# Kernel optimization log

Hardware: AMD Instinct MI355X
Metric: run time of the kernel (lower is better)

Reference implementation:

```python
import jax, jax.numpy as jnp
import numpy as np
from jax import lax

B, T, N_INPUT = 64, 2048, 257
HIDDEN = 32
N_OUTPUT = 10


def setup_inputs() -> dict:
    key = jax.random.key(0)
    ks = jax.random.split(key, 7)
    return {
        "specs": jax.random.normal(ks[0], (B, T, N_INPUT), dtype=jnp.float32),
        "W_ih": jax.random.normal(ks[1], (4 * HIDDEN, N_INPUT), dtype=jnp.float32) * 0.05,
        "W_hh": jax.random.normal(ks[2], (4 * HIDDEN, HIDDEN), dtype=jnp.float32) * 0.05,
        "b_ih": jax.random.normal(ks[3], (4 * HIDDEN,), dtype=jnp.float32) * 0.05,
        "b_hh": jax.random.normal(ks[4], (4 * HIDDEN,), dtype=jnp.float32) * 0.05,
        "W_out": jax.random.normal(ks[5], (N_OUTPUT, HIDDEN), dtype=jnp.float32) * 0.05,
        "b_out": jax.random.normal(ks[6], (N_OUTPUT,), dtype=jnp.float32) * 0.05,
    }


def reference(specs, W_ih, W_hh, b_ih, b_hh, W_out, b_out):
    # specs: [B, T, n_input]. PyTorch LSTMCell, gate order (i, f, g, o).
    b, t, _ = specs.shape
    h0 = jnp.zeros((b, HIDDEN), dtype=specs.dtype)
    c0 = jnp.zeros((b, HIDDEN), dtype=specs.dtype)
    # Precompute input projection for all timesteps in one GEMM: [B, T, 4H]
    x_proj = jnp.einsum("bti,gi->btg", specs, W_ih) + b_ih + b_hh
    x_proj = jnp.swapaxes(x_proj, 0, 1)  # [T, B, 4H] for scan

    def step(carry, xg):
        h, c = carry
        gates = xg + h @ W_hh.T  # [B, 4H]
        i, f, g, o = jnp.split(gates, 4, axis=-1)
        i = jax.nn.sigmoid(i)
        f = jax.nn.sigmoid(f)
        g = jnp.tanh(g)
        o = jax.nn.sigmoid(o)
        c = f * c + i * g
        h = o * jnp.tanh(c)
        return (h, c), None

    (hn, _), _ = lax.scan(step, (h0, c0), x_proj)
    logits = jax.nn.relu(hn) @ W_out.T + b_out  # [B, n_output]
    return jax.nn.log_softmax(logits, axis=1)
```

## Files before the change

kernel.cpp:

```cpp
#include <hip/hip_runtime.h>

#define B_SZ 64
#define T_LEN 2048
#define NIN 257
#define HID 32
#define G4 128
#define NOUT 10

#define TBT 128
#define PAD 34
#define CH 8
#define NSCAN 64
#define NGEMMP 128
#define NTILE 1024
#define TPB 16

typedef int v2i __attribute__((ext_vector_type(2)));
typedef unsigned long long u64;

__device__ __forceinline__ void pkfma2(float2& acc, float2 w, u64 h2) {
  asm("v_pk_fma_f32 %0, %1, %2, %0" : "+v"(acc) : "v"(w), "s"(h2));
}

__device__ __forceinline__ float2 pkadd(float2 a, float2 b) {
  float2 d;
  asm("v_pk_add_f32 %0, %1, %2" : "=v"(d) : "v"(a), "v"(b));
  return d;
}

#define LDP(a0, b0, PB, OA, OB) \
  asm volatile("global_load_dword %0, %2, off offset:" OA "\n\t" \
               "global_load_dword %1, %2, off offset:" OB \
               : "=&v"(a0), "=&v"(b0) : "v"(PB))

#define LOAD_CHUNK(Aa, Bb, PB) do { \
  LDP(Aa[0], Bb[0], PB, "0",    "256");  \
  LDP(Aa[1], Bb[1], PB, "512",  "768");  \
  LDP(Aa[2], Bb[2], PB, "1024", "1280"); \
  LDP(Aa[3], Bb[3], PB, "1536", "1792"); \
  LDP(Aa[4], Bb[4], PB, "2048", "2304"); \
  LDP(Aa[5], Bb[5], PB, "2560", "2816"); \
  LDP(Aa[6], Bb[6], PB, "3072", "3328"); \
  LDP(Aa[7], Bb[7], PB, "3584", "3840"); \
} while (0)

#define WAIT16() do { asm volatile("s_waitcnt vmcnt(16)" ::: "memory"); \
                      __builtin_amdgcn_sched_barrier(0); } while (0)
#define WAIT0()  do { asm volatile("s_waitcnt vmcnt(0)" ::: "memory"); \
                      __builtin_amdgcn_sched_barrier(0); } while (0)

__device__ __forceinline__ void gemm_tile(
    const float* __restrict__ A, const float* __restrict__ W,
    const float* __restrict__ b_ih, const float* __restrict__ b_hh,
    float* __restrict__ C, int bt0, float* sA, float* sB)
{
  const int tid = threadIdx.x;
  const int gt = tid & 15;
  const int btt = tid >> 4;
  float acc[8][8];
#pragma unroll
  for (int i = 0; i < 8; ++i)
#pragma unroll
    for (int j = 0; j < 8; ++j) acc[i][j] = 0.f;

  for (int kc = 0; kc < 8; ++kc) {
    const int k0 = kc * 32;
    __syncthreads();
#pragma unroll
    for (int i = 0; i < 16; ++i) {
      int s = i * 256 + tid;
      int r = s >> 5, cc = s & 31;
      sA[r * PAD + cc] = A[(size_t)(bt0 + r) * NIN + k0 + cc];
      sB[r * PAD + cc] = W[(size_t)r * NIN + k0 + cc];
    }
    __syncthreads();
#pragma unroll
    for (int k2 = 0; k2 < 16; ++k2) {
      float2 a2[8], b2[8];
#pragma unroll
      for (int i = 0; i < 8; ++i)
        a2[i] = *(const float2*)&sA[(btt + 16 * i) * PAD + 2 * k2];
#pragma unroll
      for (int j = 0; j < 8; ++j)
        b2[j] = *(const float2*)&sB[(gt + 16 * j) * PAD + 2 * k2];
#pragma unroll
      for (int i = 0; i < 8; ++i)
#pragma unroll
        for (int j = 0; j < 8; ++j) {
          acc[i][j] = fmaf(a2[i].x, b2[j].x, acc[i][j]);
          acc[i][j] = fmaf(a2[i].y, b2[j].y, acc[i][j]);
        }
    }
  }
  {
    float a[8], bb[8];
#pragma unroll
    for (int i = 0; i < 8; ++i) a[i] = A[(size_t)(bt0 + btt + 16 * i) * NIN + 256];
#pragma unroll
    for (int j = 0; j < 8; ++j) bb[j] = W[(size_t)(gt + 16 * j) * NIN + 256];
#pragma unroll
    for (int i = 0; i < 8; ++i)
#pragma unroll
      for (int j = 0; j < 8; ++j) acc[i][j] += a[i] * bb[j];
  }
  float bias[8];
#pragma unroll
  for (int j = 0; j < 8; ++j) bias[j] = b_ih[gt + 16 * j] + b_hh[gt + 16 * j];
#pragma unroll
  for (int i = 0; i < 8; ++i) {
    size_t row = (size_t)(bt0 + btt + 16 * i) * G4;
#pragma unroll
    for (int j = 0; j < 8; ++j) C[row + gt + 16 * j] = acc[i][j] + bias[j];
  }
}

__global__ __launch_bounds__(256) void fused(
    const float* __restrict__ A,
    const float* __restrict__ W,
    const float* __restrict__ b_ih,
    const float* __restrict__ b_hh,
    const float* __restrict__ W_hh,
    const float* __restrict__ W_out,
    const float* __restrict__ b_out,
    float* __restrict__ out,
    float* __restrict__ xproj,
    int* __restrict__ flags,
    int nowait)
{
  __shared__ float sA[TBT * PAD];
  __shared__ float sB[G4 * PAD];
  const int bid = blockIdx.x;

  if (bid >= NSCAN) {
    const int p = bid - NSCAN;
    for (int idx = p; idx < NTILE; idx += NGEMMP) {
      const int ti = idx >> 6, bb = idx & 63;
      const int bt0 = bb * T_LEN + ti * TBT;
      gemm_tile(A, W, b_ih, b_hh, xproj, bt0, sA, sB);
      __threadfence();
      __syncthreads();
      if (threadIdx.x == 0)
        __hip_atomic_store(&flags[idx], 1, __ATOMIC_RELEASE, __HIP_MEMORY_SCOPE_AGENT);
    }
    return;
  }

  if (threadIdx.x >= 64) return;
  __builtin_amdgcn_s_setprio(3);
  const int b = bid;
  const int l = threadIdx.x;

  float2 wA[16], wB[16];
#pragma unroll
  for (int j = 0; j < 16; j += 2) {
    float4 v0 = *(const float4*)&W_hh[l * HID + 2 * j];
    wA[j]     = make_float2(v0.x, v0.y);
    wA[j + 1] = make_float2(v0.z, v0.w);
    float4 v1 = *(const float4*)&W_hh[(l + 64) * HID + 2 * j];
    wB[j]     = make_float2(v1.x, v1.y);
    wB[j + 1] = make_float2(v1.z, v1.w);
  }
  const float eB  = (l < HID) ? -2.88539008f : -1.44269504f;
  const float mBc = (l < HID) ? 2.f : 1.f;
  const float aBc = (l < HID) ? -1.f : 0.f;

  float c = 0.f, h = 0.f;
  u64 hp[16];
#pragma unroll
  for (int k = 0; k < 16; ++k) hp[k] = 0ull;

  const float* xb = xproj + (size_t)b * T_LEN * G4;

  auto step = [&](float xa, float xg) {
    float2 aA[4], aB[4];
    aA[0] = make_float2(xa, 0.f);
    aB[0] = make_float2(xg, 0.f);
#pragma unroll
    for (int q = 1; q < 4; ++q) {
      aA[q] = make_float2(0.f, 0.f);
      aB[q] = make_float2(0.f, 0.f);
    }
#pragma unroll
    for (int j = 0; j < 16; j += 4) {
#pragma unroll
      for (int q = 0; q < 4; ++q) {
        pkfma2(aA[q], wA[j + q], hp[j + q]);
        pkfma2(aB[q], wB[j + q], hp[j + q]);
      }
    }
    float2 tA = pkadd(pkadd(aA[0], aA[1]), pkadd(aA[2], aA[3]));
    float2 tB = pkadd(pkadd(aB[0], aB[1]), pkadd(aB[2], aB[3]));
    float accA = tA.x + tA.y;
    float accB = tB.x + tB.y;
    float actA = __builtin_amdgcn_rcpf(1.f + __builtin_amdgcn_exp2f(-1.44269504f * accA));
    float sB2  = __builtin_amdgcn_rcpf(1.f + __builtin_amdgcn_exp2f(eB * accB));
    float actB = fmaf(mBc, sB2, aBc);
    float prod = actA * actB;
    v2i sw = __builtin_amdgcn_permlane32_swap(0, __float_as_int(prod), false, false);
    float pr = __int_as_float(sw[0]);
    c = fmaf(actA, c, pr);
    float t  = __builtin_amdgcn_rcpf(1.f + __builtin_amdgcn_exp2f(-2.88539008f * c));
    float o2 = actB + actB;
    h = fmaf(o2, t, -actB);
#pragma unroll
    for (int k = 0; k < 16; ++k) {
      unsigned lo = (unsigned)__builtin_amdgcn_readlane(__float_as_int(h), 32 + 2 * k);
      unsigned hi = (unsigned)__builtin_amdgcn_readlane(__float_as_int(h), 33 + 2 * k);
      hp[k] = (u64)lo | ((u64)hi << 32);
    }
  };

  float A0[CH], B0[CH], A1[CH], B1[CH];
#define STEPS(Aa, Bb) do { _Pragma("unroll") \
  for (int i = 0; i < CH; ++i) step(Aa[i], Bb[i]); } while (0)

  for (int ti = 0; ti < TPB; ++ti) {
    if (!nowait) {
      while (__hip_atomic_load(&flags[ti * 64 + b], __ATOMIC_ACQUIRE,
                               __HIP_MEMORY_SCOPE_AGENT) == 0)
        __builtin_amdgcn_s_sleep(2);
    }
    const float* pb = xb + (size_t)ti * TBT * G4 + l;
    LOAD_CHUNK(A0, B0, pb); pb += CH * G4;
    LOAD_CHUNK(A1, B1, pb); pb += CH * G4;
#pragma unroll 1
    for (int pc = 0; pc < 7; ++pc) {
      WAIT16();
      STEPS(A0, B0);
      LOAD_CHUNK(A0, B0, pb); pb += CH * G4;
      WAIT16();
      STEPS(A1, B1);
      LOAD_CHUNK(A1, B1, pb); pb += CH * G4;
    }
    WAIT16();
    STEPS(A0, B0);
    WAIT0();
    STEPS(A1, B1);
  }

  float hf[HID];
#pragma unroll
  for (int k = 0; k < HID; ++k)
    hf[k] = __int_as_float(__builtin_amdgcn_readlane(__float_as_int(h), 32 + k));
  float logit = 0.f;
  if (l < NOUT) {
    logit = b_out[l];
#pragma unroll
    for (int j = 0; j < HID; ++j) logit += fmaxf(hf[j], 0.f) * W_out[l * HID + j];
  }
  float m = -1e30f;
#pragma unroll
  for (int n = 0; n < NOUT; ++n) m = fmaxf(m, __shfl(logit, n));
  float s = 0.f;
#pragma unroll
  for (int n = 0; n < NOUT; ++n)
    s += __builtin_amdgcn_exp2f(1.44269504089f * (__shfl(logit, n) - m));
  if (l < NOUT)
    out[b * NOUT + l] = logit - m - 0.69314718056f * __builtin_amdgcn_logf(s);
}

__global__ __launch_bounds__(256) void xproj_gemm(
    const float* __restrict__ A, const float* __restrict__ W,
    const float* __restrict__ b_ih, const float* __restrict__ b_hh,
    float* __restrict__ C)
{
  __shared__ float sA[TBT * PAD];
  __shared__ float sB[G4 * PAD];
  const int idx = blockIdx.x;
  const int ti = idx >> 6, bb = idx & 63;
  gemm_tile(A, W, b_ih, b_hh, C, bb * T_LEN + ti * TBT, sA, sB);
}

extern "C" void kernel_launch(void* const* d_in, const int* in_sizes, int n_in,
                              void* d_out, int out_size, void* d_ws, size_t ws_size,
                              hipStream_t stream) {
  const float* specs = (const float*)d_in[0];
  const float* W_ih  = (const float*)d_in[1];
  const float* W_hh  = (const float*)d_in[2];
  const float* b_ih  = (const float*)d_in[3];
  const float* b_hh  = (const float*)d_in[4];
  const float* W_out = (const float*)d_in[5];
  const float* b_out = (const float*)d_in[6];
  float* outp  = (float*)d_out;
  float* xproj = (float*)d_ws;
  const size_t xbytes = (size_t)B_SZ * T_LEN * G4 * 4;

  if (ws_size >= xbytes + NTILE * sizeof(int)) {
    int* flags = (int*)((char*)d_ws + xbytes);
    (void)hipMemsetAsync(flags, 0, NTILE * sizeof(int), stream);
    fused<<<NSCAN + NGEMMP, 256, 0, stream>>>(specs, W_ih, b_ih, b_hh, W_hh,
                                              W_out, b_out, outp, xproj, flags, 0);
  } else {
    xproj_gemm<<<NTILE, 256, 0, stream>>>(specs, W_ih, b_ih, b_hh, xproj);
    fused<<<NSCAN, 256, 0, stream>>>(specs, W_ih, b_ih, b_hh, W_hh,
                                     W_out, b_out, outp, xproj, (int*)xproj , 1);
  }
}
```

Baseline: 571.8 us.

## Prescale gate preactivations and interleave xproj layout for float2 loads

The GEMM epilogue now multiplies each gate column by its sigmoid/tanh exp2 scale and stores columns interleaved so each scan lane reads its two gate values with one float2 load. The recurrent weights are prescaled the same way, which removes the per-step multiplies and the select-based tanh fixup and rewrites the cell update algebraically. The hand-written inline-asm load pipeline with explicit vmcnt waits is replaced by plain C++ double-buffered loads. The compiler may now schedule the loads and waits less tightly than the hand-tuned asm on the serial critical path.

```diff
diff --git a/kernel.cpp b/kernel.cpp
--- a/kernel.cpp
+++ b/kernel.cpp
@@ -15,6 +15,9 @@
 #define NTILE 1024
 #define TPB 16
 
+#define SC_SIG  -1.44269504f
+#define SC_TANH -2.88539008f
+
 typedef int v2i __attribute__((ext_vector_type(2)));
 typedef unsigned long long u64;
 
@@ -27,27 +30,6 @@
   asm("v_pk_add_f32 %0, %1, %2" : "=v"(d) : "v"(a), "v"(b));
   return d;
 }
-
-#define LDP(a0, b0, PB, OA, OB) \
-  asm volatile("global_load_dword %0, %2, off offset:" OA "\n\t" \
-               "global_load_dword %1, %2, off offset:" OB \
-               : "=&v"(a0), "=&v"(b0) : "v"(PB))
-
-#define LOAD_CHUNK(Aa, Bb, PB) do { \
-  LDP(Aa[0], Bb[0], PB, "0",    "256");  \
-  LDP(Aa[1], Bb[1], PB, "512",  "768");  \
-  LDP(Aa[2], Bb[2], PB, "1024", "1280"); \
-  LDP(Aa[3], Bb[3], PB, "1536", "1792"); \
-  LDP(Aa[4], Bb[4], PB, "2048", "2304"); \
-  LDP(Aa[5], Bb[5], PB, "2560", "2816"); \
-  LDP(Aa[6], Bb[6], PB, "3072", "3328"); \
-  LDP(Aa[7], Bb[7], PB, "3584", "3840"); \
-} while (0)
-
-#define WAIT16() do { asm volatile("s_waitcnt vmcnt(16)" ::: "memory"); \
-                      __builtin_amdgcn_sched_barrier(0); } while (0)
-#define WAIT0()  do { asm volatile("s_waitcnt vmcnt(0)" ::: "memory"); \
-                      __builtin_amdgcn_sched_barrier(0); } while (0)
 
 __device__ __forceinline__ void gemm_tile(
     const float* __restrict__ A, const float* __restrict__ W,
@@ -103,14 +85,20 @@
 #pragma unroll
       for (int j = 0; j < 8; ++j) acc[i][j] += a[i] * bb[j];
   }
-  float bias[8];
-#pragma unroll
-  for (int j = 0; j < 8; ++j) bias[j] = b_ih[gt + 16 * j] + b_hh[gt + 16 * j];
+  float bias[8], sc[8];
+  int off[8];
+#pragma unroll
+  for (int j = 0; j < 8; ++j) {
+    const int col = gt + 16 * j;
+    bias[j] = b_ih[col] + b_hh[col];
+    sc[j] = ((col >> 5) == 2) ? SC_TANH : SC_SIG;
+    off[j] = ((col & 63) << 1) + (col >> 6);
+  }
 #pragma unroll
   for (int i = 0; i < 8; ++i) {
     size_t row = (size_t)(bt0 + btt + 16 * i) * G4;
 #pragma unroll
-    for (int j = 0; j < 8; ++j) C[row + gt + 16 * j] = acc[i][j] + bias[j];
+    for (int j = 0; j < 8; ++j) C[row + off[j]] = (acc[i][j] + bias[j]) * sc[j];
   }
 }
 
@@ -150,26 +138,24 @@
   const int b = bid;
   const int l = threadIdx.x;
 
+  const float wsB = (l < HID) ? SC_TANH : SC_SIG;
   float2 wA[16], wB[16];
 #pragma unroll
   for (int j = 0; j < 16; j += 2) {
     float4 v0 = *(const float4*)&W_hh[l * HID + 2 * j];
-    wA[j]     = make_float2(v0.x, v0.y);
-    wA[j + 1] = make_float2(v0.z, v0.w);
+    wA[j]     = make_float2(v0.x * SC_SIG, v0.y * SC_SIG);
+    wA[j + 1] = make_float2(v0.z * SC_SIG, v0.w * SC_SIG);
     float4 v1 = *(const float4*)&W_hh[(l + 64) * HID + 2 * j];
-    wB[j]     = make_float2(v1.x, v1.y);
-    wB[j + 1] = make_float2(v1.z, v1.w);
-  }
-  const float eB  = (l < HID) ? -2.88539008f : -1.44269504f;
-  const float mBc = (l < HID) ? 2.f : 1.f;
-  const float aBc = (l < HID) ? -1.f : 0.f;
+    wB[j]     = make_float2(v1.x * wsB, v1.y * wsB);
+    wB[j + 1] = make_float2(v1.z * wsB, v1.w * wsB);
+  }
 
   float c = 0.f, h = 0.f;
   u64 hp[16];
 #pragma unroll
   for (int k = 0; k < 16; ++k) hp[k] = 0ull;
 
-  const float* xb = xproj + (size_t)b * T_LEN * G4;
+  const float2* xb2 = (const float2*)(xproj + (size_t)b * T_LEN * G4);
 
   auto step = [&](float xa, float xg) {
     float2 aA[4], aB[4];
@@ -192,16 +178,16 @@
     float2 tB = pkadd(pkadd(aB[0], aB[1]), pkadd(aB[2], aB[3]));
     float accA = tA.x + tA.y;
     float accB = tB.x + tB.y;
-    float actA = __builtin_amdgcn_rcpf(1.f + __builtin_amdgcn_exp2f(-1.44269504f * accA));
-    float sB2  = __builtin_amdgcn_rcpf(1.f + __builtin_amdgcn_exp2f(eB * accB));
-    float actB = fmaf(mBc, sB2, aBc);
-    float prod = actA * actB;
+    float actA = __builtin_amdgcn_rcpf(1.f + __builtin_amdgcn_exp2f(accA));
+    float sB2  = __builtin_amdgcn_rcpf(1.f + __builtin_amdgcn_exp2f(accB));
+    float actA2 = actA + actA;
+    float prod  = fmaf(actA2, sB2, -actA);
     v2i sw = __builtin_amdgcn_permlane32_swap(0, __float_as_int(prod), false, false);
     float pr = __int_as_float(sw[0]);
     c = fmaf(actA, c, pr);
-    float t  = __builtin_amdgcn_rcpf(1.f + __builtin_amdgcn_exp2f(-2.88539008f * c));
-    float o2 = actB + actB;
-    h = fmaf(o2, t, -actB);
+    float t  = __builtin_amdgcn_rcpf(1.f + __builtin_amdgcn_exp2f(SC_TANH * c));
+    float s2 = sB2 + sB2;
+    h = fmaf(s2, t, -sB2);
 #pragma unroll
     for (int k = 0; k < 16; ++k) {
       unsigned lo = (unsigned)__builtin_amdgcn_readlane(__float_as_int(h), 32 + 2 * k);
@@ -210,9 +196,11 @@
     }
   };
 
-  float A0[CH], B0[CH], A1[CH], B1[CH];
-#define STEPS(Aa, Bb) do { _Pragma("unroll") \
-  for (int i = 0; i < CH; ++i) step(Aa[i], Bb[i]); } while (0)
+  float2 X0[CH], X1[CH];
+#define LOADC2(X, P) do { _Pragma("unroll") \
+  for (int i = 0; i < CH; ++i) X[i] = (P)[i * 64]; } while (0)
+#define STEPS(X) do { _Pragma("unroll") \
+  for (int i = 0; i < CH; ++i) step(X[i].x, X[i].y); } while (0)
 
   for (int ti = 0; ti < TPB; ++ti) {
     if (!nowait) {
@@ -220,22 +208,19 @@
                                __HIP_MEMORY_SCOPE_AGENT) == 0)
         __builtin_amdgcn_s_sleep(2);
     }
-    const float* pb = xb + (size_t)ti * TBT * G4 + l;
-    LOAD_CHUNK(A0, B0, pb); pb += CH * G4;
-    LOAD_CHUNK(A1, B1, pb); pb += CH * G4;
+    const float2* xt = xb2 + (size_t)ti * TBT * 64 + l;
+    LOADC2(X0, xt);
 #pragma unroll 1
-    for (int pc = 0; pc < 7; ++pc) {
-      WAIT16();
-      STEPS(A0, B0);
-      LOAD_CHUNK(A0, B0, pb); pb += CH * G4;
-      WAIT16();
-      STEPS(A1, B1);
-      LOAD_CHUNK(A1, B1, pb); pb += CH * G4;
-    }
-    WAIT16();
-    STEPS(A0, B0);
-    WAIT0();
-    STEPS(A1, B1);
+    for (int ch = 0; ch < TBT / CH; ch += 2) {
+      const float2* s1 = xt + (size_t)(ch + 1) * CH * 64;
+      LOADC2(X1, s1);
+      STEPS(X0);
+      if (ch + 2 < TBT / CH) {
+        const float2* s2 = xt + (size_t)(ch + 2) * CH * 64;
+        LOADC2(X0, s2);
+      }
+      STEPS(X1);
+    }
   }
 
   float hf[HID];
```

Result: no change. 565.9 us (-1.0%).
